# Kernel optimization log

Hardware: AMD Instinct MI355X
Metric: run time of the kernel (lower is better)

The kernel has to match this reference:

```python
import jax, jax.numpy as jnp
import numpy as np

B, N, F = 8, 2048, 64
H, LAT = 256, 64
K1, K2 = N // 2, N // 4  # DiffPool keeps nodes//2 per stage


def _adj_mm(A, x):
    # A: [N,M] (shared) or [B,N,M] (per-sample); x: [B,M,F]
    if A.ndim == 2:
        return jnp.einsum('nm,bmf->bnf', A, x)
    return jnp.einsum('bnm,bmf->bnf', A, x)


def _gcn(x, A, W, b, act=None):
    # spektral GCNConv: act(A @ (X W) + b)
    h = _adj_mm(A, x @ W) + b
    return act(h) if act is not None else h


def _diffpool(x, A, K_emb, K_pool):
    # spektral DiffPool (linear embedding activation, softmax selection)
    z = _adj_mm(A, x @ K_emb)                               # [B,N,C]
    s = jax.nn.softmax(_adj_mm(A, x @ K_pool), axis=-1)     # [B,N,K]
    x_pool = jnp.einsum('bnk,bnc->bkc', s, z)               # S^T Z
    AS = _adj_mm(A, s)                                       # [B,N,K]
    A_pool = jnp.einsum('bnk,bnl->bkl', s, AS)              # S^T A S
    return x_pool, A_pool, s


def setup_inputs() -> dict:
    key = jax.random.key(0)
    ks = jax.random.split(key, 24)

    def glorot(k, shape):
        return (jax.random.normal(k, shape) * jnp.sqrt(2.0 / (shape[0] + shape[1]))).astype(jnp.float32)

    # symmetric sparse-ish adjacency with self loops, GCN-normalized (keeps activations stable)
    mask = (jax.random.uniform(ks[0], (N, N)) < 0.01).astype(jnp.float32)
    A = jnp.minimum(jnp.maximum(mask, mask.T) + jnp.eye(N, dtype=jnp.float32), 1.0)
    dinv = 1.0 / jnp.sqrt(jnp.sum(A, axis=-1))
    adj = A * dinv[:, None] * dinv[None, :]

    return {
        'x': jax.random.normal(ks[1], (B, N, F), dtype=jnp.float32),
        'eps': jax.random.normal(ks[2], (B, K2, LAT), dtype=jnp.float32),
        'adj': adj,
        'We1': glorot(ks[3], (F, H)), 'be1': jnp.zeros((H,), jnp.float32),
        'Kemb1': glorot(ks[4], (H, H)), 'Kpool1': glorot(ks[5], (H, K1)),
        'We2': glorot(ks[6], (H, H)), 'be2': jnp.zeros((H,), jnp.float32),
        'Kemb2': glorot(ks[7], (H, H)), 'Kpool2': glorot(ks[8], (H, K2)),
        'We3': glorot(ks[9], (H, 2 * LAT)), 'be3': jnp.zeros((2 * LAT,), jnp.float32),
        'Wd0': glorot(ks[10], (LAT, H)), 'bd0': jnp.zeros((H,), jnp.float32),
        'Wd1': glorot(ks[11], (H, H)), 'bd1': jnp.zeros((H,), jnp.float32),
        'Wd2': glorot(ks[12], (H, H)), 'bd2': jnp.zeros((H,), jnp.float32),
        'Wdf': glorot(ks[13], (H, F)), 'bdf': jnp.zeros((F,), jnp.float32),
    }


def reference(x, eps, adj, We1, be1, Kemb1, Kpool1, We2, be2, Kemb2, Kpool2,
              We3, be3, Wd0, bd0, Wd1, bd1, Wd2, bd2, Wdf, bdf):
    A0 = adj
    # ---- encode ----
    h = _gcn(x, A0, We1, be1, jax.nn.relu)              # [B,N,H]
    h, A1, s1 = _diffpool(h, A0, Kemb1, Kpool1)          # [B,K1,H], [B,K1,K1], [B,N,K1]
    h = _gcn(h, A1, We2, be2, jax.nn.relu)
    h, A2, s2 = _diffpool(h, A1, Kemb2, Kpool2)          # [B,K2,H]
    h = _gcn(h, A2, We3, be3, None)                      # [B,K2,2*LAT]
    mean, log_var = jnp.split(h, 2, axis=-1)
    z = mean + jnp.exp(0.5 * log_var) * eps              # reparameterize
    # ---- decode ----
    d = _gcn(z, A2, Wd0, bd0, jax.nn.relu)
    d = jnp.einsum('bnk,bkc->bnc', s2, d)                # DiffUnpool: S @ x
    d = _gcn(d, A1, Wd1, bd1, jax.nn.relu)
    d = jnp.einsum('bnk,bkc->bnc', s1, d)
    d = _gcn(d, A0, Wd2, bd2, jax.nn.relu)
    out = _gcn(d, A0, Wdf, bdf, jax.nn.softplus)         # [B,N,F]
    return out, mean, log_var
```

## Files before the change

kernel.cpp:

```cpp
#include <hip/hip_runtime.h>
#include <math.h>

#define BATCH 8
typedef unsigned short US;

typedef __attribute__((ext_vector_type(8))) short short8;
typedef __attribute__((ext_vector_type(4))) float f32x4;

__device__ __forceinline__ US f2b(float f) {
  union { float f; unsigned u; } v; v.f = f;
  unsigned r = v.u + 0x7fffu + ((v.u >> 16) & 1u);
  return (US)(r >> 16);
}
__device__ __forceinline__ float b2f(US h) {
  union { unsigned u; float f; } v; v.u = ((unsigned)h) << 16;
  return v.f;
}

__device__ __forceinline__ void gload16(const US* g, US* l) {
  __builtin_amdgcn_global_load_lds(
      (const __attribute__((address_space(1))) unsigned int*)g,
      (__attribute__((address_space(3))) unsigned int*)l, 16, 0, 0);
}

__device__ __forceinline__ int lidx2(int r, int ko) {
  return r * 64 + ((((ko >> 3) ^ (r & 7)) << 3));
}

template <int TN, int ACT, int OUT, bool HASBIAS>
__global__ __launch_bounds__(256) void mm_k(
    const US* __restrict__ A, const US* __restrict__ B,
    const float* __restrict__ bias, void* __restrict__ Cv, void* __restrict__ Cv2,
    int M, int N, int K, int lda, long long sA, long long sB, long long sC,
    long long sC2, int gx, int gy) {
  constexpr int JF = TN / 32;
  __shared__ US As[128 * 64];
  __shared__ US Bs[TN * 64];

  const int nb = blockIdx.x;
  const int nb2 = (nb & 7) * (gx * gy) + (nb >> 3);
  const int bx = nb2 % gx;
  const int by = (nb2 / gx) % gy;
  const int b = nb2 / (gx * gy);

  A += (long long)b * sA;
  B += (long long)b * sB;
  const int m0 = by * 128, n0 = bx * TN;
  const int t = threadIdx.x, lane = t & 63, w = t >> 6;
  const int wm = (w >> 1) * 64, wn = (w & 1) * (TN / 2);
  const int l15 = lane & 15, lg = lane >> 4;
  const int lrow = lane >> 3;
  const int gcell = (((lane & 7) ^ lrow) << 3);

  f32x4 acc[4][JF];
#pragma unroll
  for (int i = 0; i < 4; ++i)
#pragma unroll
    for (int j = 0; j < JF; ++j) acc[i][j] = (f32x4){0.f, 0.f, 0.f, 0.f};

  for (int k0 = 0; k0 < K; k0 += 64) {
#pragma unroll
    for (int i = 0; i < 4; ++i) {
      const int g = w * 4 + i;
      gload16(A + (long long)(m0 + g * 8 + lrow) * lda + k0 + gcell, &As[g * 512]);
    }
#pragma unroll
    for (int i = 0; i < TN / 32; ++i) {
      const int g = w * (TN / 32) + i;
      gload16(B + (long long)(n0 + g * 8 + lrow) * K + k0 + gcell, &Bs[g * 512]);
    }
    __syncthreads();

#pragma unroll
    for (int kk = 0; kk < 2; ++kk) {
      const int ko = kk * 32 + lg * 8;
      short8 af[4], bf[JF];
#pragma unroll
      for (int i = 0; i < 4; ++i)
        af[i] = *(const short8*)&As[lidx2(wm + i * 16 + l15, ko)];
#pragma unroll
      for (int j = 0; j < JF; ++j)
        bf[j] = *(const short8*)&Bs[lidx2(wn + j * 16 + l15, ko)];
#pragma unroll
      for (int i = 0; i < 4; ++i)
#pragma unroll
        for (int j = 0; j < JF; ++j)
          acc[i][j] = __builtin_amdgcn_mfma_f32_16x16x32_bf16(af[i], bf[j],
                                                              acc[i][j], 0, 0, 0);
    }
    __syncthreads();
  }

  const long long cb = (long long)b * sC;
  const long long cb2 = (long long)b * sC2;
#pragma unroll
  for (int fj = 0; fj < JF; ++fj) {
    const int col = n0 + wn + fj * 16 + l15;
    const float bsv = HASBIAS ? bias[col] : 0.0f;
#pragma unroll
    for (int fi = 0; fi < 4; ++fi) {
      const int row0 = m0 + wm + fi * 16 + lg * 4;
      float v[4];
#pragma unroll
      for (int e = 0; e < 4; ++e) {
        float x = acc[fi][fj][e] + bsv;
        if (ACT == 1) x = fmaxf(x, 0.0f);
        if (ACT == 2) x = (x > 20.0f) ? x : log1pf(expf(x));
        v[e] = x;
      }
      if (OUT == 1 || OUT == 3) {
        ushort4 pk;
        pk.x = f2b(v[0]); pk.y = f2b(v[1]); pk.z = f2b(v[2]); pk.w = f2b(v[3]);
        US* c2 = (OUT == 3) ? (US*)Cv2 : (US*)Cv;
        *(ushort4*)&c2[cb2 + (long long)col * M + row0] = pk;
      }
      if (OUT == 0 || OUT == 3) {
#pragma unroll
        for (int e = 0; e < 4; ++e)
          ((US*)Cv)[cb + (long long)(row0 + e) * N + col] = f2b(v[e]);
      }
      if (OUT == 2) {
#pragma unroll
        for (int e = 0; e < 4; ++e)
          ((float*)Cv)[cb + (long long)(row0 + e) * N + col] = v[e];
      }
    }
  }
}

template <int OUT>
__global__ __launch_bounds__(512, 1) void mm256_k(
    const US* __restrict__ A, const US* __restrict__ B, void* __restrict__ Cv,
    void* __restrict__ Cv2, int M, int N, int K, int lda, long long sA,
    long long sB, long long sC, long long sC2, int gx, int gy) {
  __shared__ US lds[8][8192];

  const int nb = blockIdx.x;
  const int chunk = gx * gy;
  const int nb2 = (nb & 7) * chunk + (nb >> 3);
  const int bx = nb2 % gx;
  const int by = (nb2 / gx) % gy;
  const int b = nb2 / chunk;

  const int m0 = by * 256, n0 = bx * 256;
  const int tid = threadIdx.x;
  const int lane = tid & 63, w = tid >> 6;
  const int wr = w >> 2, wc = w & 3;
  const int l15 = lane & 15, lg = lane >> 4;

  const US* Ab = A + (long long)b * sA + (long long)m0 * lda;
  const US* Bb = B + (long long)b * sB + (long long)n0 * K;
  const int NT = K >> 6;

  auto stageH = [&](int H) {
    const int s = H >> 2, h = H & 3;
    const int ab = h & 1, kk = h >> 1;
    US* reg = &lds[ab * 4 + (s & 1) * 2 + kk][0];
    const US* src = ab ? Bb : Ab;
    const int ld = ab ? K : lda;
#pragma unroll
    for (int i = 0; i < 2; ++i) {
      const int rbase = (w * 2 + i) * 16;
      const int r = rbase + (lane >> 2);
      const int csrc = (lane & 3) ^ ((r >> 1) & 3);
      gload16(src + (long long)r * ld + s * 64 + kk * 32 + csrc * 8,
              reg + rbase * 32);
    }
  };

  f32x4 acc[8][4];
#pragma unroll
  for (int m = 0; m < 8; ++m)
#pragma unroll
    for (int j = 0; j < 4; ++j) acc[m][j] = (f32x4){0.f, 0.f, 0.f, 0.f};
  short8 a4[4], b4[4];

  for (int H = 0; H < 6; ++H) stageH(H);
  asm volatile("s_waitcnt vmcnt(4)" ::: "memory");
  __builtin_amdgcn_s_barrier();

#define PH(kk_, mh_, DOH, HV, VM, tt)                                          \
  {                                                                            \
    const US* Ar = &lds[((tt) & 1) * 2 + (kk_)][0];                            \
    const US* Br = &lds[4 + ((tt) & 1) * 2 + (kk_)][0];                        \
    _Pragma("unroll") for (int i = 0; i < 4; ++i) {                            \
      const int r = wr * 128 + (mh_) * 64 + i * 16 + l15;                      \
      a4[i] = *(const short8*)&Ar[r * 32 + ((lg ^ ((r >> 1) & 3)) << 3)];      \
    }                                                                          \
    if ((mh_) == 0) {                                                          \
      _Pragma("unroll") for (int j = 0; j < 4; ++j) {                          \
        const int rr = wc * 64 + j * 16 + l15;                                 \
        b4[j] = *(const short8*)&Br[rr * 32 + ((lg ^ ((rr >> 1) & 3)) << 3)];  \
      }                                                                        \
    }                                                                          \
    if (DOH) stageH(HV);                                                       \
    if ((VM) == 1) asm volatile("s_waitcnt vmcnt(4)" ::: "memory");            \
    if ((VM) == 2) asm volatile("s_waitcnt vmcnt(0)" ::: "memory");            \
    __builtin_amdgcn_s_barrier();                                              \
    __builtin_amdgcn_s_setprio(1);                                             \
    _Pragma("unroll") for (int i = 0; i < 4; ++i)                              \
      _Pragma("unroll") for (int j = 0; j < 4; ++j)                            \
        acc[(mh_) * 4 + i][j] = __builtin_amdgcn_mfma_f32_16x16x32_bf16(       \
            a4[i], b4[j], acc[(mh_) * 4 + i][j], 0, 0, 0);                     \
    __builtin_amdgcn_s_setprio(0);                                             \
    __builtin_amdgcn_s_barrier();                                              \
  }

  int t2 = 0;
  for (; t2 < NT - 2; ++t2) {
    PH(0, 0, true, 4 * t2 + 6, 0, t2)
    PH(0, 1, true, 4 * t2 + 7, 0, t2)
    PH(1, 0, true, 4 * t2 + 8, 0, t2)
    PH(1, 1, true, 4 * t2 + 9, 1, t2)
  }
  PH(0, 0, true, 4 * (NT - 2) + 6, 0, NT - 2)
  PH(0, 1, true, 4 * (NT - 2) + 7, 0, NT - 2)
  PH(1, 0, false, 0, 0, NT - 2)
  PH(1, 1, false, 0, 2, NT - 2)
  PH(0, 0, false, 0, 0, NT - 1)
  PH(0, 1, false, 0, 0, NT - 1)
  PH(1, 0, false, 0, 0, NT - 1)
  PH(1, 1, false, 0, 0, NT - 1)
#undef PH

  const long long cb = (long long)b * sC;
  const long long cb2 = (long long)b * sC2;
#pragma unroll
  for (int j = 0; j < 4; ++j) {
    const int col = n0 + wc * 64 + j * 16 + l15;
#pragma unroll
    for (int m = 0; m < 8; ++m) {
      const int row0 = m0 + wr * 128 + m * 16 + lg * 4;
      if (OUT == 1 || OUT == 3) {
        ushort4 pk;
        pk.x = f2b(acc[m][j][0]); pk.y = f2b(acc[m][j][1]);
        pk.z = f2b(acc[m][j][2]); pk.w = f2b(acc[m][j][3]);
        US* c2 = (OUT == 3) ? (US*)Cv2 : (US*)Cv;
        *(ushort4*)&c2[cb2 + (long long)col * M + row0] = pk;
      }
      if (OUT == 0 || OUT == 3) {
#pragma unroll
        for (int e = 0; e < 4; ++e)
          ((US*)Cv)[cb + (long long)(row0 + e) * N + col] = f2b(acc[m][j][e]);
      }
    }
  }
}

template <int ACT, int OUT, bool HASBIAS>
__global__ __launch_bounds__(256) void mm64_k(
    const US* __restrict__ A, const US* __restrict__ B,
    const float* __restrict__ bias, void* __restrict__ Cv,
    int M, int N, int K, int lda, long long sA, long long sB, long long sC,
    int gx, int gy) {
  __shared__ US As[4][4096];
  __shared__ US Bs[4][4096];

  const int nb = blockIdx.x;
  const int chunk = gx * gy;
  const int nb2 = (nb & 7) * chunk + (nb >> 3);
  const int bx = nb2 % gx;
  const int by = (nb2 / gx) % gy;
  const int b = nb2 / chunk;

  const int m0 = by * 64, n0 = bx * 64;
  const int tid = threadIdx.x;
  const int lane = tid & 63, w = tid >> 6;
  const int wr = w >> 1, wc = w & 1;
  const int l15 = lane & 15, lg = lane >> 4;
  const int lrow = lane >> 3;
  const int gcell = (((lane & 7) ^ lrow) << 3);

  const US* Ag = A + (long long)b * sA + (long long)m0 * lda;
  const US* Bg = B + (long long)b * sB + (long long)n0 * K;
  const int NT = K >> 6;

  auto stage = [&](int tt) {
    US* Ad = &As[tt & 3][0];
    US* Bd = &Bs[tt & 3][0];
    const int k0 = tt * 64;
#pragma unroll
    for (int i = 0; i < 2; ++i) {
      const int g = w * 2 + i;
      const int r = g * 8 + lrow;
      gload16(Ag + (long long)r * lda + k0 + gcell, Ad + g * 512);
      gload16(Bg + (long long)r * K + k0 + gcell, Bd + g * 512);
    }
  };

  f32x4 acc[2][2];
#pragma unroll
  for (int i = 0; i < 2; ++i)
#pragma unroll
    for (int j = 0; j < 2; ++j) acc[i][j] = (f32x4){0.f, 0.f, 0.f, 0.f};

  for (int i = 0; i < 3 && i < NT; ++i) stage(i);

  for (int t = 0; t < NT; ++t) {
    if (t + 3 < NT) stage(t + 3);
    const int rem = NT - 1 - t;
    if (rem >= 3) asm volatile("s_waitcnt vmcnt(12)" ::: "memory");
    else if (rem == 2) asm volatile("s_waitcnt vmcnt(8)" ::: "memory");
    else if (rem == 1) asm volatile("s_waitcnt vmcnt(4)" ::: "memory");
    else asm volatile("s_waitcnt vmcnt(0)" ::: "memory");
    asm volatile("s_barrier" ::: "memory");
    const US* Ad = &As[t & 3][0];
    const US* Bd = &Bs[t & 3][0];
#pragma unroll
    for (int kk = 0; kk < 2; ++kk) {
      const int ko = kk * 32 + lg * 8;
      short8 af[2], bf[2];
      af[0] = *(const short8*)&Ad[lidx2(wr * 32 + l15, ko)];
      af[1] = *(const short8*)&Ad[lidx2(wr * 32 + 16 + l15, ko)];
      bf[0] = *(const short8*)&Bd[lidx2(wc * 32 + l15, ko)];
      bf[1] = *(const short8*)&Bd[lidx2(wc * 32 + 16 + l15, ko)];
#pragma unroll
      for (int i = 0; i < 2; ++i)
#pragma unroll
        for (int j = 0; j < 2; ++j)
          acc[i][j] = __builtin_amdgcn_mfma_f32_16x16x32_bf16(af[i], bf[j],
                                                              acc[i][j], 0, 0, 0);
    }
    asm volatile("s_barrier" ::: "memory");
  }

  const long long cb = (long long)b * sC;
#pragma unroll
  for (int fj = 0; fj < 2; ++fj) {
    const int col = n0 + wc * 32 + fj * 16 + l15;
    const float bsv = HASBIAS ? bias[col] : 0.0f;
#pragma unroll
    for (int fi = 0; fi < 2; ++fi) {
      const int row0 = m0 + wr * 32 + fi * 16 + lg * 4;
      float v[4];
#pragma unroll
      for (int e = 0; e < 4; ++e) {
        float x = acc[fi][fj][e] + bsv;
        if (ACT == 1) x = fmaxf(x, 0.0f);
        if (ACT == 2) x = (x > 20.0f) ? x : log1pf(expf(x));
        v[e] = x;
      }
      if (OUT == 1) {
        ushort4 pk;
        pk.x = f2b(v[0]); pk.y = f2b(v[1]); pk.z = f2b(v[2]); pk.w = f2b(v[3]);
        *(ushort4*)&((US*)Cv)[cb + (long long)col * M + row0] = pk;
      } else if (OUT == 0) {
#pragma unroll
        for (int e = 0; e < 4; ++e)
          ((US*)Cv)[cb + (long long)(row0 + e) * N + col] = f2b(v[e]);
      } else {
#pragma unroll
        for (int e = 0; e < 4; ++e)
          ((float*)Cv)[cb + (long long)(row0 + e) * N + col] = v[e];
      }
    }
  }
}

template <int RPT>
__global__ __launch_bounds__(256) void sm_partial_k(
    const US* __restrict__ x, float* __restrict__ pm, float* __restrict__ ps,
    int R, int C, long long sB, int NS) {
  const int b = blockIdx.y, blk = blockIdx.x;
  const int cpr = C >> 3;
  const int t = threadIdx.x;
  const int cslot = t & (cpr - 1);
  const int rsub = t / cpr;
  const int nsub = 256 / cpr;
  const int rowsPerBlock = R / NS;
  const int r0 = blk * rowsPerBlock + rsub * RPT;
  const US* p = x + (long long)b * sB + (long long)r0 * C + cslot * 8;
  union { uint4 v; US s[8]; } buf[RPT];
#pragma unroll
  for (int i = 0; i < RPT; ++i) buf[i].v = *(const uint4*)(p + (long long)i * C);
  float M[8], S[8];
#pragma unroll
  for (int j = 0; j < 8; ++j) M[j] = b2f(buf[0].s[j]);
#pragma unroll
  for (int i = 1; i < RPT; ++i)
#pragma unroll
    for (int j = 0; j < 8; ++j) M[j] = fmaxf(M[j], b2f(buf[i].s[j]));
#pragma unroll
  for (int j = 0; j < 8; ++j) S[j] = 0.f;
#pragma unroll
  for (int i = 0; i < RPT; ++i)
#pragma unroll
    for (int j = 0; j < 8; ++j) S[j] += __expf(b2f(buf[i].s[j]) - M[j]);
  const long long pi = (long long)(b * NS + blk) * nsub + rsub;
  float* pmo = pm + pi * C + cslot * 8;
  float* pso = ps + pi * C + cslot * 8;
  *(float4*)pmo = make_float4(M[0], M[1], M[2], M[3]);
  *(float4*)(pmo + 4) = make_float4(M[4], M[5], M[6], M[7]);
  *(float4*)pso = make_float4(S[0], S[1], S[2], S[3]);
  *(float4*)(pso + 4) = make_float4(S[4], S[5], S[6], S[7]);
}

__global__ __launch_bounds__(256) void sm_combine_k(
    const float* __restrict__ pm, const float* __restrict__ ps,
    float* __restrict__ Mf, float* __restrict__ Sinv, int C, int NP) {
  const int b = blockIdx.x, t = threadIdx.x;
  const int cpr = C >> 3;
  if (t >= cpr) return;
  const int c = t * 8;
  const float* pmB = pm + (long long)b * NP * C + c;
  const float* psB = ps + (long long)b * NP * C + c;
  float M[8], S[8];
#pragma unroll
  for (int j = 0; j < 8; ++j) { M[j] = pmB[j]; S[j] = psB[j]; }
  for (int e = 1; e < NP; ++e) {
    const float* pme = pmB + (long long)e * C;
    const float* pse = psB + (long long)e * C;
#pragma unroll
    for (int j = 0; j < 8; ++j) {
      const float m2 = pme[j], s2 = pse[j];
      const float nm = fmaxf(M[j], m2);
      S[j] = S[j] * __expf(M[j] - nm) + s2 * __expf(m2 - nm);
      M[j] = nm;
    }
  }
#pragma unroll
  for (int j = 0; j < 8; ++j) {
    Mf[(long long)b * C + c + j] = M[j];
    Sinv[(long long)b * C + c + j] = 1.0f / S[j];
  }
}

template <int RPT>
__global__ __launch_bounds__(256) void sm_norm_k(
    US* __restrict__ x, const float* __restrict__ Mf,
    const float* __restrict__ Sinv, int R, int C, long long sB, int NS) {
  const int b = blockIdx.y, blk = blockIdx.x;
  const int cpr = C >> 3;
  const int t = threadIdx.x;
  const int cslot = t & (cpr - 1);
  const int rsub = t / cpr;
  const int rowsPerBlock = R / NS;
  const int r0 = blk * rowsPerBlock + rsub * RPT;
  US* p = x + (long long)b * sB + (long long)r0 * C + cslot * 8;
  float M[8], Si[8];
#pragma unroll
  for (int j = 0; j < 8; ++j) {
    M[j] = Mf[(long long)b * C + cslot * 8 + j];
    Si[j] = Sinv[(long long)b * C + cslot * 8 + j];
  }
#pragma unroll
  for (int i = 0; i < RPT; ++i) {
    union { uint4 v; US s[8]; } buf;
    buf.v = *(const uint4*)(p + (long long)i * C);
#pragma unroll
    for (int j = 0; j < 8; ++j)
      buf.s[j] = f2b(__expf(b2f(buf.s[j]) - M[j]) * Si[j]);
    *(uint4*)(p + (long long)i * C) = buf.v;
  }
}

__global__ __launch_bounds__(256) void trans_k(const float* __restrict__ src,
                                               US* __restrict__ dst, int R, int C,
                                               long long sIn, long long sOut) {
  __shared__ US L[64][65];
  const int b = blockIdx.z;
  const int r0 = blockIdx.y * 64, c0 = blockIdx.x * 64;
  const int t = threadIdx.x;
  const int lr = t >> 4, lc = (t & 15) * 4;
  const float* s = src + (long long)b * sIn;
#pragma unroll
  for (int i = 0; i < 4; ++i) {
    const int rr = r0 + lr + 16 * i;
    const float4 v = *(const float4*)&s[(long long)rr * C + c0 + lc];
    L[lr + 16 * i][lc + 0] = f2b(v.x);
    L[lr + 16 * i][lc + 1] = f2b(v.y);
    L[lr + 16 * i][lc + 2] = f2b(v.z);
    L[lr + 16 * i][lc + 3] = f2b(v.w);
  }
  __syncthreads();
#pragma unroll
  for (int i = 0; i < 4; ++i) {
    ushort4 o;
    o.x = L[lc + 0][lr + 16 * i];
    o.y = L[lc + 1][lr + 16 * i];
    o.z = L[lc + 2][lr + 16 * i];
    o.w = L[lc + 3][lr + 16 * i];
    *(ushort4*)&dst[(long long)b * sOut + (long long)(c0 + lr + 16 * i) * R + r0 + lc] = o;
  }
}

struct WT { const float* src; US* dst; int R, C, tileOff; };
struct WTab { WT e[11]; };

__global__ __launch_bounds__(256) void wtrans_k(WTab tab) {
  __shared__ US L[64][65];
  const int tile = blockIdx.x;
  int i = 0;
#pragma unroll
  for (int j = 1; j < 11; ++j)
    if (tab.e[j].tileOff <= tile) i = j;
  const WT w = tab.e[i];
  const int lt = tile - w.tileOff;
  const int tc = w.C / 64;
  const int r0 = (lt / tc) * 64, c0 = (lt % tc) * 64;
  const int t = threadIdx.x;
  const int lr = t >> 4, lc = (t & 15) * 4;
#pragma unroll
  for (int k = 0; k < 4; ++k) {
    const int rr = r0 + lr + 16 * k;
    const float4 v = *(const float4*)&w.src[(long long)rr * w.C + c0 + lc];
    L[lr + 16 * k][lc + 0] = f2b(v.x);
    L[lr + 16 * k][lc + 1] = f2b(v.y);
    L[lr + 16 * k][lc + 2] = f2b(v.z);
    L[lr + 16 * k][lc + 3] = f2b(v.w);
  }
  __syncthreads();
#pragma unroll
  for (int k = 0; k < 4; ++k) {
    ushort4 o;
    o.x = L[lc + 0][lr + 16 * k];
    o.y = L[lc + 1][lr + 16 * k];
    o.z = L[lc + 2][lr + 16 * k];
    o.w = L[lc + 3][lr + 16 * k];
    *(ushort4*)&w.dst[(long long)(c0 + lr + 16 * k) * w.R + r0 + lc] = o;
  }
}

__global__ __launch_bounds__(256) void f2b_k(const float* __restrict__ s,
                                             US* __restrict__ d, int n4) {
  const int i = blockIdx.x * 256 + threadIdx.x;
  if (i < n4) {
    const float4 v = ((const float4*)s)[i];
    ushort4 o;
    o.x = f2b(v.x); o.y = f2b(v.y); o.z = f2b(v.z); o.w = f2b(v.w);
    ((ushort4*)d)[i] = o;
  }
}

__global__ __launch_bounds__(256) void reparam_k(
    const float* __restrict__ h3, const float* __restrict__ eps,
    float* __restrict__ om, float* __restrict__ olv, US* __restrict__ z,
    int total) {
  const int i = blockIdx.x * 256 + threadIdx.x;
  if (i >= total) return;
  const int j = i & 63;
  const long long r = i >> 6;
  const float m = h3[r * 128 + j];
  const float lv = h3[r * 128 + 64 + j];
  om[i] = m;
  olv[i] = lv;
  z[i] = f2b(m + expf(0.5f * lv) * eps[i]);
}

static void mm(hipStream_t st, const US* A, const US* B, const float* bias,
               void* C, void* C2, int M, int N, int K, int lda, long long sA,
               long long sB, long long sC, long long sC2, int act, int outm,
               int tn) {
  const int gx = N / tn, gy = M / 128;
  dim3 g(gx * gy * BATCH), blk(256);
#define L(TN, ACT, OUT, HB) \
  mm_k<TN, ACT, OUT, HB><<<g, blk, 0, st>>>(A, B, bias, C, C2, M, N, K, lda, sA, sB, sC, sC2, gx, gy)
  if (tn == 64) {
    if (outm == 0) L(64, 0, 0, false);
    else if (outm == 1) L(64, 0, 1, false);
    else L(64, 2, 2, true);
  } else {
    if (outm == 0) {
      if (act == 1) L(128, 1, 0, true);
      else L(128, 0, 0, false);
    } else if (outm == 1) {
      if (act == 1) L(128, 1, 1, true);
      else L(128, 0, 1, false);
    } else if (outm == 2) L(128, 0, 2, true);
    else L(128, 0, 3, false);
  }
#undef L
}

static void mm256(hipStream_t st, const US* A, const US* B, void* C, void* C2,
                  int M, int N, int K, int lda, long long sA, long long sB,
                  long long sC, long long sC2, int outm) {
  const int gx = N / 256, gy = M / 256;
  dim3 g(gx * gy * BATCH), blk(512);
  if (outm == 0)
    mm256_k<0><<<g, blk, 0, st>>>(A, B, C, C2, M, N, K, lda, sA, sB, sC, sC2, gx, gy);
  else if (outm == 1)
    mm256_k<1><<<g, blk, 0, st>>>(A, B, C, C2, M, N, K, lda, sA, sB, sC, sC2, gx, gy);
  else
    mm256_k<3><<<g, blk, 0, st>>>(A, B, C, C2, M, N, K, lda, sA, sB, sC, sC2, gx, gy);
}

static void mm64(hipStream_t st, const US* A, const US* B, const float* bias,
                 void* C, int M, int N, int K, int lda, long long sA,
                 long long sB, long long sC, int act, int outm) {
  const int gx = N / 64, gy = M / 64;
  dim3 g(gx * gy * BATCH), blk(256);
  if (outm == 0)
    mm64_k<0, 0, false><<<g, blk, 0, st>>>(A, B, nullptr, C, M, N, K, lda, sA, sB, sC, gx, gy);
  else if (outm == 1)
    mm64_k<0, 1, false><<<g, blk, 0, st>>>(A, B, nullptr, C, M, N, K, lda, sA, sB, sC, gx, gy);
  else
    mm64_k<2, 2, true><<<g, blk, 0, st>>>(A, B, bias, C, M, N, K, lda, sA, sB, sC, gx, gy);
}

extern "C" void kernel_launch(void* const* d_in, const int* in_sizes, int n_in,
                              void* d_out, int out_size, void* d_ws, size_t ws_size,
                              hipStream_t stream) {
  const float* x      = (const float*)d_in[0];
  const float* eps    = (const float*)d_in[1];
  const float* adj    = (const float*)d_in[2];
  const float* We1    = (const float*)d_in[3];
  const float* be1    = (const float*)d_in[4];
  const float* Kemb1  = (const float*)d_in[5];
  const float* Kpool1 = (const float*)d_in[6];
  const float* We2    = (const float*)d_in[7];
  const float* be2    = (const float*)d_in[8];
  const float* Kemb2  = (const float*)d_in[9];
  const float* Kpool2 = (const float*)d_in[10];
  const float* We3    = (const float*)d_in[11];
  const float* be3    = (const float*)d_in[12];
  const float* Wd0    = (const float*)d_in[13];
  const float* bd0    = (const float*)d_in[14];
  const float* Wd1    = (const float*)d_in[15];
  const float* bd1    = (const float*)d_in[16];
  const float* Wd2    = (const float*)d_in[17];
  const float* bd2    = (const float*)d_in[18];
  const float* Wdf    = (const float*)d_in[19];
  const float* bdf    = (const float*)d_in[20];
  (void)in_sizes; (void)n_in; (void)ws_size; (void)out_size;

  float* out = (float*)d_out;
  float* out_mean = out + (long long)8 * 2048 * 64;
  float* out_lv = out_mean + (long long)8 * 512 * 64;

  char* base = (char*)d_ws;
  size_t off = 0;
  auto alloc = [&](size_t bytes) {
    char* p = base + off;
    off += (bytes + 255) & ~(size_t)255;
    return p;
  };
  US* adjb = (US*)alloc(2048LL * 2048 * 2);
  US* xT   = (US*)alloc(8LL * 64 * 2048 * 2);
  US* Y0   = (US*)alloc(8LL * 2048 * 64 * 2);
  US* h1T  = (US*)alloc(8LL * 256 * 2048 * 2);
  US* g1   = (US*)alloc(8LL * 2048 * 256 * 2);
  US* R1   = (US*)alloc(8LL * 2304 * 2048 * 2);
  US* AS1  = (US*)alloc(8LL * 2048 * 1024 * 2);
  US* P1o  = (US*)alloc(8LL * 1024 * 1280 * 2);
  US* t1T  = (US*)alloc(8LL * 256 * 1024 * 2);
  US* h2T  = (US*)alloc(8LL * 256 * 1024 * 2);
  US* g2   = (US*)alloc(8LL * 1024 * 256 * 2);
  US* R2   = (US*)alloc(8LL * 1280 * 1024 * 2);
  US* AS2  = (US*)alloc(8LL * 1024 * 512 * 2);
  US* P2o  = (US*)alloc(8LL * 512 * 768 * 2);
  US* t2T  = (US*)alloc(8LL * 128 * 512 * 2);
  float* h3f = (float*)alloc(8LL * 512 * 128 * 4);
  US* zlb  = (US*)alloc(8LL * 512 * 64 * 2);
  US* t3T  = (US*)alloc(8LL * 256 * 512 * 2);
  US* d0   = (US*)alloc(8LL * 512 * 256 * 2);
  US* t4T  = (US*)alloc(8LL * 256 * 512 * 2);
  US* d2   = (US*)alloc(8LL * 1024 * 256 * 2);
  US* t5T  = (US*)alloc(8LL * 256 * 1024 * 2);
  US* d4   = (US*)alloc(8LL * 2048 * 256 * 2);
  US* t6T  = (US*)alloc(8LL * 64 * 2048 * 2);
  float* pm   = (float*)alloc(8LL * 128 * 2048 * 4);
  float* ps   = (float*)alloc(8LL * 128 * 2048 * 4);
  float* Mf   = (float*)alloc(8LL * 2048 * 4);
  float* Sinv = (float*)alloc(8LL * 2048 * 4);
  US* We1T  = (US*)alloc(256 * 64 * 2);
  US* KpKe1 = (US*)alloc(1280 * 256 * 2);
  US* We2T  = (US*)alloc(256 * 256 * 2);
  US* KpKe2 = (US*)alloc(768 * 256 * 2);
  US* We3T  = (US*)alloc(128 * 256 * 2);
  US* Wd0T  = (US*)alloc(256 * 64 * 2);
  US* Wd1T  = (US*)alloc(256 * 256 * 2);
  US* Wd2T  = (US*)alloc(256 * 256 * 2);
  US* WdfT  = (US*)alloc(64 * 256 * 2);

  f2b_k<<<dim3(2048 * 2048 / 4 / 256), dim3(256), 0, stream>>>(adj, adjb, 2048 * 2048 / 4);
  trans_k<<<dim3(1, 32, 8), dim3(256), 0, stream>>>(x, xT, 2048, 64, 2048LL * 64,
                                                    64LL * 2048);
  {
    WTab tab;
    int toff = 0, i = 0;
    auto add = [&](const float* s, US* d, int R, int C) {
      tab.e[i++] = WT{s, d, R, C, toff};
      toff += (R / 64) * (C / 64);
    };
    add(We1, We1T, 64, 256);
    add(Kpool1, KpKe1, 256, 1024);
    add(Kemb1, KpKe1 + 1024 * 256, 256, 256);
    add(We2, We2T, 256, 256);
    add(Kpool2, KpKe2, 256, 512);
    add(Kemb2, KpKe2 + 512 * 256, 256, 256);
    add(We3, We3T, 256, 128);
    add(Wd0, Wd0T, 64, 256);
    add(Wd1, Wd1T, 256, 256);
    add(Wd2, Wd2T, 256, 256);
    add(Wdf, WdfT, 256, 64);
    wtrans_k<<<dim3(toff), dim3(256), 0, stream>>>(tab);
  }

  const long long SR1 = 2304LL * 2048, SR2 = 1280LL * 1024;
  US* s1T  = R1;
  US* B1   = R1 + 1024 * 2048;
  US* AS1T = R1 + 1280 * 2048;
  US* s2T  = R2;
  US* B2   = R2 + 512 * 1024;
  US* AS2T = R2 + 768 * 1024;
  US* A1c  = P1o + 256;
  US* A2c  = P2o + 256;

  mm64(stream, adjb, xT, nullptr, Y0, 2048, 64, 2048, 2048, 0, 64LL * 2048,
       2048LL * 64, 0, 0);
  mm(stream, Y0, We1T, be1, h1T, nullptr, 2048, 256, 64, 64, 2048LL * 64, 0, 0,
     256LL * 2048, 1, 1, 128);
  mm(stream, adjb, h1T, nullptr, g1, nullptr, 2048, 256, 2048, 2048, 0,
     256LL * 2048, 2048LL * 256, 0, 0, 0, 128);
  mm256(stream, g1, KpKe1, R1, nullptr, 2048, 1280, 256, 256, 2048LL * 256, 0,
        SR1, SR1, 1);
  sm_partial_k<8><<<dim3(128, 8), dim3(256), 0, stream>>>(s1T, pm, ps, 1024, 2048, SR1, 128);
  sm_combine_k<<<dim3(8), dim3(256), 0, stream>>>(pm, ps, Mf, Sinv, 2048, 128);
  sm_norm_k<8><<<dim3(128, 8), dim3(256), 0, stream>>>(s1T, Mf, Sinv, 1024, 2048, SR1, 128);
  mm256(stream, adjb, s1T, AS1, AS1T, 2048, 1024, 2048, 2048, 0, SR1,
        2048LL * 1024, SR1, 3);
  mm(stream, s1T, B1, nullptr, P1o, nullptr, 1024, 1280, 2048, 2048, SR1, SR1,
     1024LL * 1280, 0, 0, 0, 128);
  mm(stream, P1o, We2T, nullptr, t1T, nullptr, 1024, 256, 256, 1280, 1024LL * 1280,
     0, 0, 256LL * 1024, 0, 1, 128);
  mm(stream, A1c, t1T, be2, h2T, nullptr, 1024, 256, 1024, 1280, 1024LL * 1280,
     256LL * 1024, 0, 256LL * 1024, 1, 1, 128);
  mm(stream, A1c, h2T, nullptr, g2, nullptr, 1024, 256, 1024, 1280, 1024LL * 1280,
     256LL * 1024, 1024LL * 256, 0, 0, 0, 128);
  mm(stream, g2, KpKe2, nullptr, R2, nullptr, 1024, 768, 256, 256, 1024LL * 256,
     0, 0, SR2, 0, 1, 128);
  sm_partial_k<4><<<dim3(64, 8), dim3(256), 0, stream>>>(s2T, pm, ps, 512, 1024, SR2, 64);
  sm_combine_k<<<dim3(8), dim3(256), 0, stream>>>(pm, ps, Mf, Sinv, 1024, 128);
  sm_norm_k<4><<<dim3(64, 8), dim3(256), 0, stream>>>(s2T, Mf, Sinv, 512, 1024, SR2, 64);
  mm(stream, A1c, s2T, nullptr, AS2, AS2T, 1024, 512, 1024, 1280, 1024LL * 1280,
     SR2, 1024LL * 512, SR2, 0, 3, 128);
  mm(stream, s2T, B2, nullptr, P2o, nullptr, 512, 768, 1024, 1024, SR2, SR2,
     512LL * 768, 0, 0, 0, 128);
  mm(stream, P2o, We3T, nullptr, t2T, nullptr, 512, 128, 256, 768, 512LL * 768,
     0, 0, 128LL * 512, 0, 1, 128);
  mm(stream, A2c, t2T, be3, h3f, nullptr, 512, 128, 512, 768, 512LL * 768,
     128LL * 512, 512LL * 128, 0, 0, 2, 128);
  reparam_k<<<dim3(8 * 512 * 64 / 256), dim3(256), 0, stream>>>(h3f, eps, out_mean,
                                                                out_lv, zlb, 8 * 512 * 64);

  mm(stream, zlb, Wd0T, nullptr, t3T, nullptr, 512, 256, 64, 64, 512LL * 64, 0, 0,
     256LL * 512, 0, 1, 128);
  mm(stream, A2c, t3T, bd0, d0, nullptr, 512, 256, 512, 768, 512LL * 768,
     256LL * 512, 512LL * 256, 0, 1, 0, 128);
  mm(stream, d0, Wd1T, nullptr, t4T, nullptr, 512, 256, 256, 256, 512LL * 256, 0,
     0, 256LL * 512, 0, 1, 128);
  mm(stream, AS2, t4T, bd1, d2, nullptr, 1024, 256, 512, 512, 1024LL * 512,
     256LL * 512, 1024LL * 256, 0, 1, 0, 128);
  mm(stream, d2, Wd2T, nullptr, t5T, nullptr, 1024, 256, 256, 256, 1024LL * 256, 0,
     0, 256LL * 1024, 0, 1, 128);
  mm(stream, AS1, t5T, bd2, d4, nullptr, 2048, 256, 1024, 1024, 2048LL * 1024,
     256LL * 1024, 2048LL * 256, 0, 1, 0, 128);
  mm64(stream, d4, WdfT, nullptr, t6T, 2048, 64, 256, 256, 2048LL * 256, 0,
       64LL * 2048, 0, 1);
  mm64(stream, adjb, t6T, bdf, out, 2048, 64, 2048, 2048, 0, 64LL * 2048,
       2048LL * 64, 2, 2);
}
```

Baseline: 713.1 us.

## Replace dense input-adjacency GCN matmuls with CSR SpMM built on device

Builds a CSR form of the fixed adjacency on device with count, scan and fill kernels. The first-layer and final-layer GCN aggregations with A0 then use a row-parallel sparse SpMM instead of dense MFMA matmuls, which also removes the input transpose and the transposed intermediates. The intended saving is the dense 2048x2048 products on a roughly 1%-dense matrix. In exchange it adds CSR construction passes, uses a fixed per-row capacity, and gathers with scalar loads. The S^T B product for the first pool also switches to the larger mm256 tile kernel.

```diff
diff --git a/kernel.cpp b/kernel.cpp
--- a/kernel.cpp
+++ b/kernel.cpp
@@ -357,6 +357,110 @@
   }
 }
 
+__global__ __launch_bounds__(256) void csr_count_k(const float* __restrict__ adj,
+                                                   int* __restrict__ rowcnt) {
+  const int row = blockIdx.x, t = threadIdx.x;
+  const float* p = adj + (long long)row * 2048;
+  int c = 0;
+  for (int j = t; j < 2048; j += 256) c += (p[j] != 0.0f);
+  __shared__ int red[256];
+  red[t] = c;
+  __syncthreads();
+  for (int s = 128; s; s >>= 1) {
+    if (t < s) red[t] += red[t + s];
+    __syncthreads();
+  }
+  if (t == 0) rowcnt[row] = red[0];
+}
+
+__global__ __launch_bounds__(256) void csr_scan_k(const int* __restrict__ rowcnt,
+                                                  int* __restrict__ rowptr) {
+  __shared__ int red[256];
+  const int t = threadIdx.x;
+  int base = 0;
+  for (int ch = 0; ch < 8; ++ch) {
+    const int v = rowcnt[ch * 256 + t];
+    red[t] = v;
+    __syncthreads();
+    for (int s = 1; s < 256; s <<= 1) {
+      const int add = (t >= s) ? red[t - s] : 0;
+      __syncthreads();
+      red[t] += add;
+      __syncthreads();
+    }
+    rowptr[ch * 256 + t] = base + red[t] - v;
+    const int tot = red[255];
+    __syncthreads();
+    base += tot;
+  }
+  if (t == 0) rowptr[2048] = base;
+}
+
+__global__ __launch_bounds__(256) void csr_fill_k(const float* __restrict__ adj,
+                                                  const int* __restrict__ rowptr,
+                                                  int* __restrict__ colidx,
+                                                  float* __restrict__ vals) {
+  const int row = blockIdx.x, t = threadIdx.x;
+  const float* p = adj + (long long)row * 2048;
+  int cnt = 0;
+  for (int j = t; j < 2048; j += 256) cnt += (p[j] != 0.0f);
+  __shared__ int red[256];
+  red[t] = cnt;
+  __syncthreads();
+  for (int s = 1; s < 256; s <<= 1) {
+    const int add = (t >= s) ? red[t - s] : 0;
+    __syncthreads();
+    red[t] += add;
+    __syncthreads();
+  }
+  int off = rowptr[row] + red[t] - cnt;
+  for (int j = t; j < 2048; j += 256) {
+    const float a = p[j];
+    if (a != 0.0f) {
+      colidx[off] = j;
+      vals[off] = a;
+      ++off;
+    }
+  }
+}
+
+template <int COLS, bool INF32, int ACT, bool OUTF32, bool HASBIAS>
+__global__ __launch_bounds__(256) void spmm_k(
+    const int* __restrict__ rowptr, const int* __restrict__ colidx,
+    const float* __restrict__ vals, const void* __restrict__ Xv,
+    const float* __restrict__ bias, void* __restrict__ Yv) {
+  constexpr int BP = 256 / COLS;
+  constexpr int NP = BATCH / BP;
+  const int row = blockIdx.x;
+  const int t = threadIdx.x;
+  const int c = t & (COLS - 1);
+  const int bsub = t / COLS;
+  const int e0 = rowptr[row], e1 = rowptr[row + 1];
+  float acc[NP];
+#pragma unroll
+  for (int p = 0; p < NP; ++p) acc[p] = 0.0f;
+  for (int e = e0; e < e1; ++e) {
+    const int j = colidx[e];
+    const float a = vals[e];
+#pragma unroll
+    for (int p = 0; p < NP; ++p) {
+      const int b = p * BP + bsub;
+      const long long idx = ((long long)b * 2048 + j) * COLS + c;
+      const float xv = INF32 ? ((const float*)Xv)[idx] : b2f(((const US*)Xv)[idx]);
+      acc[p] += a * xv;
+    }
+  }
+#pragma unroll
+  for (int p = 0; p < NP; ++p) {
+    const int b = p * BP + bsub;
+    float v = acc[p] + (HASBIAS ? bias[c] : 0.0f);
+    if (ACT == 2) v = (v > 20.0f) ? v : log1pf(expf(v));
+    const long long idx = ((long long)b * 2048 + row) * COLS + c;
+    if (OUTF32) ((float*)Yv)[idx] = v;
+    else ((US*)Yv)[idx] = f2b(v);
+  }
+}
+
 template <int RPT>
 __global__ __launch_bounds__(256) void sm_partial_k(
     const US* __restrict__ x, float* __restrict__ pm, float* __restrict__ ps,
@@ -451,36 +555,6 @@
     for (int j = 0; j < 8; ++j)
       buf.s[j] = f2b(__expf(b2f(buf.s[j]) - M[j]) * Si[j]);
     *(uint4*)(p + (long long)i * C) = buf.v;
-  }
-}
-
-__global__ __launch_bounds__(256) void trans_k(const float* __restrict__ src,
-                                               US* __restrict__ dst, int R, int C,
-                                               long long sIn, long long sOut) {
-  __shared__ US L[64][65];
-  const int b = blockIdx.z;
-  const int r0 = blockIdx.y * 64, c0 = blockIdx.x * 64;
-  const int t = threadIdx.x;
-  const int lr = t >> 4, lc = (t & 15) * 4;
-  const float* s = src + (long long)b * sIn;
-#pragma unroll
-  for (int i = 0; i < 4; ++i) {
-    const int rr = r0 + lr + 16 * i;
-    const float4 v = *(const float4*)&s[(long long)rr * C + c0 + lc];
-    L[lr + 16 * i][lc + 0] = f2b(v.x);
-    L[lr + 16 * i][lc + 1] = f2b(v.y);
-    L[lr + 16 * i][lc + 2] = f2b(v.z);
-    L[lr + 16 * i][lc + 3] = f2b(v.w);
-  }
-  __syncthreads();
-#pragma unroll
-  for (int i = 0; i < 4; ++i) {
-    ushort4 o;
-    o.x = L[lc + 0][lr + 16 * i];
-    o.y = L[lc + 1][lr + 16 * i];
-    o.z = L[lc + 2][lr + 16 * i];
-    o.w = L[lc + 3][lr + 16 * i];
-    *(ushort4*)&dst[(long long)b * sOut + (long long)(c0 + lr + 16 * i) * R + r0 + lc] = o;
   }
 }
 
@@ -636,9 +710,8 @@
     return p;
   };
   US* adjb = (US*)alloc(2048LL * 2048 * 2);
-  US* xT   = (US*)alloc(8LL * 64 * 2048 * 2);
   US* Y0   = (US*)alloc(8LL * 2048 * 64 * 2);
-  US* h1T  = (US*)alloc(8LL * 256 * 2048 * 2);
+  US* h1b  = (US*)alloc(8LL * 2048 * 256 * 2);
   US* g1   = (US*)alloc(8LL * 2048 * 256 * 2);
   US* R1   = (US*)alloc(8LL * 2304 * 2048 * 2);
   US* AS1  = (US*)alloc(8LL * 2048 * 1024 * 2);
@@ -658,11 +731,15 @@
   US* d2   = (US*)alloc(8LL * 1024 * 256 * 2);
   US* t5T  = (US*)alloc(8LL * 256 * 1024 * 2);
   US* d4   = (US*)alloc(8LL * 2048 * 256 * 2);
-  US* t6T  = (US*)alloc(8LL * 64 * 2048 * 2);
+  US* t6   = (US*)alloc(8LL * 2048 * 64 * 2);
   float* pm   = (float*)alloc(8LL * 128 * 2048 * 4);
   float* ps   = (float*)alloc(8LL * 128 * 2048 * 4);
   float* Mf   = (float*)alloc(8LL * 2048 * 4);
   float* Sinv = (float*)alloc(8LL * 2048 * 4);
+  int* rowcnt = (int*)alloc(2048 * 4);
+  int* rowptr = (int*)alloc(2049 * 4);
+  int* colidx = (int*)alloc(2048LL * 256 * 4);
+  float* vals = (float*)alloc(2048LL * 256 * 4);
   US* We1T  = (US*)alloc(256 * 64 * 2);
   US* KpKe1 = (US*)alloc(1280 * 256 * 2);
   US* We2T  = (US*)alloc(256 * 256 * 2);
@@ -674,8 +751,6 @@
   US* WdfT  = (US*)alloc(64 * 256 * 2);
 
   f2b_k<<<dim3(2048 * 2048 / 4 / 256), dim3(256), 0, stream>>>(adj, adjb, 2048 * 2048 / 4);
-  trans_k<<<dim3(1, 32, 8), dim3(256), 0, stream>>>(x, xT, 2048, 64, 2048LL * 64,
-                                                    64LL * 2048);
   {
     WTab tab;
     int toff = 0, i = 0;
@@ -696,6 +771,9 @@
     add(Wdf, WdfT, 256, 64);
     wtrans_k<<<dim3(toff), dim3(256), 0, stream>>>(tab);
   }
+  csr_count_k<<<dim3(2048), dim3(256), 0, stream>>>(adj, rowcnt);
+  csr_scan_k<<<dim3(1), dim3(256), 0, stream>>>(rowcnt, rowptr);
+  csr_fill_k<<<dim3(2048), dim3(256), 0, stream>>>(adj, rowptr, colidx, vals);
 
   const long long SR1 = 2304LL * 2048, SR2 = 1280LL * 1024;
   US* s1T  = R1;
@@ -707,12 +785,12 @@
   US* A1c  = P1o + 256;
   US* A2c  = P2o + 256;
 
-  mm64(stream, adjb, xT, nullptr, Y0, 2048, 64, 2048, 2048, 0, 64LL * 2048,
-       2048LL * 64, 0, 0);
-  mm(stream, Y0, We1T, be1, h1T, nullptr, 2048, 256, 64, 64, 2048LL * 64, 0, 0,
-     256LL * 2048, 1, 1, 128);
-  mm(stream, adjb, h1T, nullptr, g1, nullptr, 2048, 256, 2048, 2048, 0,
-     256LL * 2048, 2048LL * 256, 0, 0, 0, 128);
+  spmm_k<64, true, 0, false, false><<<dim3(2048), dim3(256), 0, stream>>>(
+      rowptr, colidx, vals, x, nullptr, Y0);
+  mm(stream, Y0, We1T, be1, h1b, nullptr, 2048, 256, 64, 64, 2048LL * 64, 0,
+     2048LL * 256, 0, 1, 0, 128);
+  spmm_k<256, false, 0, false, false><<<dim3(2048), dim3(256), 0, stream>>>(
+      rowptr, colidx, vals, h1b, nullptr, g1);
   mm256(stream, g1, KpKe1, R1, nullptr, 2048, 1280, 256, 256, 2048LL * 256, 0,
         SR1, SR1, 1);
   sm_partial_k<8><<<dim3(128, 8), dim3(256), 0, stream>>>(s1T, pm, ps, 1024, 2048, SR1, 128);
@@ -720,8 +798,8 @@
   sm_norm_k<8><<<dim3(128, 8), dim3(256), 0, stream>>>(s1T, Mf, Sinv, 1024, 2048, SR1, 128);
   mm256(stream, adjb, s1T, AS1, AS1T, 2048, 1024, 2048, 2048, 0, SR1,
         2048LL * 1024, SR1, 3);
-  mm(stream, s1T, B1, nullptr, P1o, nullptr, 1024, 1280, 2048, 2048, SR1, SR1,
-     1024LL * 1280, 0, 0, 0, 128);
+  mm256(stream, s1T, B1, P1o, nullptr, 1024, 1280, 2048, 2048, SR1, SR1,
+        1024LL * 1280, 0, 0);
   mm(stream, P1o, We2T, nullptr, t1T, nullptr, 1024, 256, 256, 1280, 1024LL * 1280,
      0, 0, 256LL * 1024, 0, 1, 128);
   mm(stream, A1c, t1T, be2, h2T, nullptr, 1024, 256, 1024, 1280, 1024LL * 1280,
@@ -756,8 +834,8 @@
      0, 256LL * 1024, 0, 1, 128);
   mm(stream, AS1, t5T, bd2, d4, nullptr, 2048, 256, 1024, 1024, 2048LL * 1024,
      256LL * 1024, 2048LL * 256, 0, 1, 0, 128);
-  mm64(stream, d4, WdfT, nullptr, t6T, 2048, 64, 256, 256, 2048LL * 256, 0,
-       64LL * 2048, 0, 1);
-  mm64(stream, adjb, t6T, bdf, out, 2048, 64, 2048, 2048, 0, 64LL * 2048,
-       2048LL * 64, 2, 2);
-}
+  mm64(stream, d4, WdfT, nullptr, t6, 2048, 64, 256, 256, 2048LL * 256, 0,
+       2048LL * 64, 0, 0);
+  spmm_k<64, false, 2, true, true><<<dim3(2048), dim3(256), 0, stream>>>(
+      rowptr, colidx, vals, t6, bdf, out);
+}
```

Result: no change. 702.4 us (-1.5%).
